# Kernel optimization log

Hardware: AMD Instinct MI355X
Metric: run time of the kernel (lower is better)

Reference implementation:

```python
import jax, jax.numpy as jnp
import numpy as np

B, C, H, W, NH = 16, 384, 28, 28, 6
S = H * W
EPS = 1e-5
SCALE = C ** -0.5  # note: original scales by dim**-0.5, not head_dim**-0.5


def setup_inputs():
    key = jax.random.key(0)
    ks = jax.random.split(key, 5)
    return {
        "x1": jax.random.normal(ks[0], (B, S, C), jnp.float32),
        "h1": H, "w1": W,
        "x2": jax.random.normal(ks[1], (B, S, C), jnp.float32),
        "h2": H, "w2": W,
        # stacked params for the 9 conv branches: q1,k1,v1,q2,k2,v2,q3,k3,v3
        "dw_w": jax.random.normal(ks[2], (9, C, 1, 3, 3), jnp.float32) * 0.1,
        "bn_gamma": jnp.ones((9, C), jnp.float32),
        "bn_beta": jnp.zeros((9, C), jnp.float32),
        "pw_w": jax.random.normal(ks[3], (9, C, C), jnp.float32) * (C ** -0.5),
        "pw_b": jnp.zeros((9, C), jnp.float32),
        "lin_w": jax.random.normal(ks[4], (9, C, C), jnp.float32) * (C ** -0.5),
    }


def _conv_branch(img, dw, g, b, pw, pwb):
    # depthwise 3x3 conv (no bias) -> train-mode BatchNorm2d -> 1x1 conv (bias)
    y = jax.lax.conv_general_dilated(
        img, dw, (1, 1), ((1, 1), (1, 1)),
        feature_group_count=img.shape[1],
        dimension_numbers=('NCHW', 'OIHW', 'NCHW'))
    mu = y.mean(axis=(0, 2, 3), keepdims=True)
    var = ((y - mu) ** 2).mean(axis=(0, 2, 3), keepdims=True)  # biased var, like torch BN
    y = (y - mu) * jax.lax.rsqrt(var + EPS) * g[None, :, None, None] + b[None, :, None, None]
    y = jnp.einsum('bchw,oc->bohw', y, pw) + pwb[None, :, None, None]
    return y.reshape(y.shape[0], y.shape[1], -1).transpose(0, 2, 1)  # b (h w) c


def _heads(x, w):
    # Linear (no bias): y = x @ w.T, then 'b t (h d) -> b h t d'
    y = jnp.einsum('btc,oc->bto', x, w)
    b, t, c = y.shape
    return y.reshape(b, t, NH, c // NH).transpose(0, 2, 1, 3)


def _attn(q, k, v):
    s = jnp.einsum('bhld,bhtd->bhlt', q, k) * SCALE
    a = jax.nn.softmax(s, axis=-1)
    o = jnp.einsum('bhlt,bhtd->bhld', a, v)
    b, h, t, d = o.shape
    # NOTE: original torch does .view(b, t, h*d) on a (b,h,t,d) tensor WITHOUT
    # transposing heads next to depth; replicate that raw reshape exactly.
    return o.reshape(b, t, h * d)


def _forward(x1, h1, w1, x2, h2, w2, dw_w, bn_gamma, bn_beta, pw_w, pw_b, lin_w):
    b, _, c = x1.shape
    i1 = x1.reshape(b, h1, w1, c).transpose(0, 3, 1, 2)  # b c h w
    i2 = x2.reshape(b, h2, w2, c).transpose(0, 3, 1, 2)
    i3 = i1 + i2
    imgs = (i1, i2, i3)
    outs = []
    for br in range(3):
        q = _conv_branch(imgs[br], dw_w[3*br+0], bn_gamma[3*br+0], bn_beta[3*br+0], pw_w[3*br+0], pw_b[3*br+0])
        k = _conv_branch(imgs[br], dw_w[3*br+1], bn_gamma[3*br+1], bn_beta[3*br+1], pw_w[3*br+1], pw_b[3*br+1])
        v = _conv_branch(imgs[br], dw_w[3*br+2], bn_gamma[3*br+2], bn_beta[3*br+2], pw_w[3*br+2], pw_b[3*br+2])
        # branch 3 reuses branch-2 Linear weights (bug in original source, replicated)
        li = 3 if br == 2 else 3 * br
        outs.append(_attn(_heads(q, lin_w[li+0]), _heads(k, lin_w[li+1]), _heads(v, lin_w[li+2])))
    return tuple(outs)


def reference(x1, h1, w1, x2, h2, w2, dw_w, bn_gamma, bn_beta, pw_w, pw_b, lin_w):
    return _forward(x1, h1, w1, x2, h2, w2, dw_w, bn_gamma, bn_beta, pw_w, pw_b, lin_w)
```

## Files before the change

kernel.cpp:

```cpp
#include <hip/hip_runtime.h>

typedef unsigned short u16;
typedef unsigned int u32;
typedef unsigned long long u64;

#define B_   16
#define C_   384
#define H_   28
#define W_   28
#define S_   784
#define NH_  6
#define HD_  64
#define BS_  (B_ * S_)
#define SCALE_ 0.05103103630798288f
#define LSC_   0.07362225484151387f
#define EPS_ 1e-5f

typedef __attribute__((ext_vector_type(8))) short bf16x8;
typedef __attribute__((ext_vector_type(4))) float f32x4;

__device__ __forceinline__ float bf2f(u16 u) {
    return __uint_as_float(((u32)u) << 16);
}
__device__ __forceinline__ u16 f2bf(float f) {
    u32 x = __float_as_uint(f);
    u32 r = (x + 0x7fffu + ((x >> 16) & 1u)) >> 16;
    return (u16)r;
}

__device__ __forceinline__ void gld16(const u16* g, u16* l) {
    __builtin_amdgcn_global_load_lds(
        (__attribute__((address_space(1))) void*)g,
        (__attribute__((address_space(3))) void*)l, 16, 0, 0);
}

__device__ __forceinline__ float exp2_fast(float x) {
    float r;
    asm("v_exp_f32 %0, %1" : "=v"(r) : "v"(x));
    return r;
}

__launch_bounds__(128)
__global__ void k_conv(const float* __restrict__ x1, const float* __restrict__ x2,
                       const float* __restrict__ dw, u16* __restrict__ y,
                       float* __restrict__ part) {
    int id = blockIdx.x;
    int xcd = id & 7;
    int r = id >> 3;
    int cc = r % 3;
    int rr = r / 3;
    int p = xcd + 8 * (rr / 28);
    int h = rr % 28;
    int g = p / 16;
    int b = p % 16;
    int c = cc * 128 + threadIdx.x;

    const float* pa = x1 + (size_t)b * S_ * C_ + c;
    const float* pb = x2 + (size_t)b * S_ * C_ + c;
    float s0 = (g == 1) ? 0.f : 1.f;
    float s1 = (g == 0) ? 0.f : 1.f;

    float wt[3][9];
#pragma unroll
    for (int i = 0; i < 3; ++i)
#pragma unroll
        for (int t = 0; t < 9; ++t)
            wt[i][t] = dw[((3 * g + i) * C_ + c) * 9 + t];

    float rm[3];
    size_t ro[3];
#pragma unroll
    for (int dh = 0; dh < 3; ++dh) {
        int hh = h + dh - 1;
        rm[dh] = (hh >= 0 && hh < H_) ? 1.f : 0.f;
        int hc = hh < 0 ? 0 : (hh > H_ - 1 ? H_ - 1 : hh);
        ro[dh] = (size_t)(hc * W_) * C_;
    }

    float a[3][3];
#pragma unroll
    for (int dh = 0; dh < 3; ++dh) {
        a[dh][0] = 0.f;
        a[dh][1] = (pa[ro[dh]] * s0 + pb[ro[dh]] * s1) * rm[dh];
        a[dh][2] = (pa[ro[dh] + C_] * s0 + pb[ro[dh] + C_] * s1) * rm[dh];
    }

    u16* dst[3];
#pragma unroll
    for (int i = 0; i < 3; ++i)
        dst[i] = y + ((size_t)((3 * g + i) * B_ + b) * S_ + h * W_) * C_ + c;

    float sum[3] = {0.f, 0.f, 0.f}, sq[3] = {0.f, 0.f, 0.f};

#pragma unroll 4
    for (int w = 0; w < W_; ++w) {
        int wn = w + 2;
        float wm = (wn < W_) ? 1.f : 0.f;
        int wc = (wn < W_) ? wn : (W_ - 1);
        size_t o0 = ro[0] + (size_t)wc * C_;
        size_t o1 = ro[1] + (size_t)wc * C_;
        size_t o2 = ro[2] + (size_t)wc * C_;
        float la0 = pa[o0], lb0 = pb[o0];
        float la1 = pa[o1], lb1 = pb[o1];
        float la2 = pa[o2], lb2 = pb[o2];
        float nx0 = (la0 * s0 + lb0 * s1) * (rm[0] * wm);
        float nx1 = (la1 * s0 + lb1 * s1) * (rm[1] * wm);
        float nx2 = (la2 * s0 + lb2 * s1) * (rm[2] * wm);

#pragma unroll
        for (int i = 0; i < 3; ++i) {
            const float* W9 = wt[i];
            float acc = a[0][0]*W9[0] + a[0][1]*W9[1] + a[0][2]*W9[2]
                      + a[1][0]*W9[3] + a[1][1]*W9[4] + a[1][2]*W9[5]
                      + a[2][0]*W9[6] + a[2][1]*W9[7] + a[2][2]*W9[8];
            sum[i] += acc;
            sq[i] = fmaf(acc, acc, sq[i]);
            dst[i][w * C_] = f2bf(acc);
        }
        a[0][0] = a[0][1]; a[0][1] = a[0][2]; a[0][2] = nx0;
        a[1][0] = a[1][1]; a[1][1] = a[1][2]; a[1][2] = nx1;
        a[2][0] = a[2][1]; a[2][1] = a[2][2]; a[2][2] = nx2;
    }
#pragma unroll
    for (int i = 0; i < 3; ++i) {
        atomicAdd(&part[((3 * g + i) * C_ + c) * 2],     sum[i]);
        atomicAdd(&part[((3 * g + i) * C_ + c) * 2 + 1], sq[i]);
    }
}

__global__ void k_wcomb(const float* __restrict__ pw, const float* __restrict__ pwb,
                        const float* __restrict__ lin,
                        const float* __restrict__ part,
                        const float* __restrict__ gamma, const float* __restrict__ beta,
                        u16* __restrict__ Wcb, float* __restrict__ Bc) {
    __shared__ float red[8];
    int id = blockIdx.x;
    int xcd = id & 7;
    int k2 = id >> 3;
    int idx, og;
    if (k2 < 96) { idx = xcd; og = k2; }
    else         { idx = 8;   og = xcd * 12 + (k2 - 96); }
    int c = threadIdx.x;
    int wave = c >> 6, lane = c & 63;
    int li = (idx < 3) ? idx : 3 + (idx % 3);

    float s_ = part[(idx * C_ + c) * 2];
    float q_ = part[(idx * C_ + c) * 2 + 1];
    float mean = s_ / (float)BS_;
    float var  = q_ / (float)BS_ - mean * mean;
    float aS = gamma[idx * C_ + c] * rsqrtf(var + EPS_);
    float bS = beta[idx * C_ + c] - mean * aS;

    float acc[4];
#pragma unroll
    for (int k = 0; k < 4; ++k) acc[k] = 0.f;
    const float* pwm = pw + (idx * C_) * C_ + c;
    const float* lb  = lin + ((li * C_) + og * 4) * C_;

    float pvv[8];
#pragma unroll
    for (int u = 0; u < 8; ++u) pvv[u] = pwm[u * C_];
    for (int m0 = 0; m0 < C_; m0 += 8) {
        float pvn[8];
        if (m0 + 8 < C_) {
#pragma unroll
            for (int u = 0; u < 8; ++u) pvn[u] = pwm[(m0 + 8 + u) * C_];
        } else {
#pragma unroll
            for (int u = 0; u < 8; ++u) pvn[u] = 0.f;
        }
#pragma unroll
        for (int u = 0; u < 8; ++u) {
            float pv = pvv[u];
#pragma unroll
            for (int k = 0; k < 4; ++k)
                acc[k] += lb[k * C_ + (m0 + u)] * pv;
        }
#pragma unroll
        for (int u = 0; u < 8; ++u) pvv[u] = pvn[u];
    }

    float pwbc = pwb[idx * C_ + c];
    for (int k = 0; k < 4; ++k) {
        int o = og * 4 + k;
        Wcb[(idx * C_ + o) * C_ + c] = f2bf(acc[k] * aS);
        float v = acc[k] * bS + lin[(li * C_ + o) * C_ + c] * pwbc;
#pragma unroll
        for (int msk = 1; msk < 64; msk <<= 1) v += __shfl_xor(v, msk);
        if (lane == 0) red[wave] = v;
        __syncthreads();
        if (c == 0)
            Bc[idx * C_ + o] = red[0] + red[1] + red[2] + red[3] + red[4] + red[5];
        __syncthreads();
    }
}

__launch_bounds__(256)
__global__ void k_gemm(const u16* __restrict__ y, const u16* __restrict__ Wcb,
                       const float* __restrict__ Bc, u16* __restrict__ qkv) {
    __shared__ __align__(16) u16 ldsA[2][4096];
    __shared__ __align__(16) u16 ldsB[2][4096];

    int id = blockIdx.x;
    int xcd = id & 7;
    int kb = id >> 3;
    int zz = kb / 21;
    int t  = kb % 21;
    int z  = zz * 8 + xcd;
    int by = t / 7, bx = t % 7;
    int idx = z >> 4, b = z & 15;

    int tid = threadIdx.x;
    int wave = tid >> 6;
    int lane = tid & 63;
    int lq = lane & 15;
    int quad = lane >> 4;
    int o_base = by * 128 + (wave & 1) * 64;
    int s_base_w = bx * 128 + (wave >> 1) * 64;

    const u16* ybase = y + (size_t)(idx * B_ + b) * S_ * C_;
    const u16* wbase = Wcb + (size_t)idx * C_ * C_;

    int r0 = tid >> 2;
    int qs = (tid & 3) ^ ((r0 ^ (r0 >> 2)) & 3);
    int srA0 = bx * 128 + r0;       if (srA0 > S_ - 1) srA0 = S_ - 1;
    int srA1 = bx * 128 + r0 + 64;  if (srA1 > S_ - 1) srA1 = S_ - 1;
    const u16* gA0 = ybase + (size_t)srA0 * C_ + qs * 8;
    const u16* gA1 = ybase + (size_t)srA1 * C_ + qs * 8;
    const u16* gB0 = wbase + (size_t)(by * 128 + r0) * C_ + qs * 8;
    const u16* gB1 = wbase + (size_t)(by * 128 + r0 + 64) * C_ + qs * 8;
    int lo0 = wave * 512;
    int lo1 = 2048 + wave * 512;

#define STAGE(stg, kk) do {                          \
        gld16(gA0 + (kk) * 32, &ldsA[stg][lo0]);     \
        gld16(gA1 + (kk) * 32, &ldsA[stg][lo1]);     \
        gld16(gB0 + (kk) * 32, &ldsB[stg][lo0]);     \
        gld16(gB1 + (kk) * 32, &ldsB[stg][lo1]);     \
    } while (0)

    f32x4 acc[4][4];
#pragma unroll
    for (int i = 0; i < 4; ++i)
#pragma unroll
        for (int j = 0; j < 4; ++j) acc[i][j] = (f32x4){0.f,0.f,0.f,0.f};

    STAGE(0, 0);
    __syncthreads();

    int qoff = (quad ^ ((lq ^ (lq >> 2)) & 3)) * 8;
    bf16x8 af[4], bw[4];
#pragma unroll
    for (int ks = 0; ks < 12; ++ks) {
        int cur = ks & 1;
        if (ks < 11) STAGE(cur ^ 1, ks + 1);
#pragma unroll
        for (int mt = 0; mt < 4; ++mt) {
            int sl = (wave >> 1) * 64 + mt * 16 + lq;
            __builtin_memcpy(&af[mt], &ldsA[cur][sl * 32 + qoff], 16);
        }
#pragma unroll
        for (int nt = 0; nt < 4; ++nt) {
            int ol = (wave & 1) * 64 + nt * 16 + lq;
            __builtin_memcpy(&bw[nt], &ldsB[cur][ol * 32 + qoff], 16);
        }
#pragma unroll
        for (int mt = 0; mt < 4; ++mt)
#pragma unroll
            for (int nt = 0; nt < 4; ++nt)
                acc[mt][nt] = __builtin_amdgcn_mfma_f32_16x16x32_bf16(
                    af[mt], bw[nt], acc[mt][nt], 0, 0, 0);
        __syncthreads();
    }
#undef STAGE

    float bias[4];
#pragma unroll
    for (int nt = 0; nt < 4; ++nt) bias[nt] = Bc[idx * C_ + o_base + nt * 16 + lq];
    u16* obase = qkv + ((size_t)(idx * B_ + b) * S_) * C_;
#pragma unroll
    for (int mt = 0; mt < 4; ++mt) {
#pragma unroll
        for (int r = 0; r < 4; ++r) {
            int s = s_base_w + mt * 16 + quad * 4 + r;
            if (s >= S_) continue;
            u16* row = obase + (size_t)s * C_ + o_base + lq;
#pragma unroll
            for (int nt = 0; nt < 4; ++nt)
                row[nt * 16] = f2bf(acc[mt][nt][r] + bias[nt]);
        }
    }
}

__launch_bounds__(256, 4)
__global__ void k_attn(const u16* __restrict__ qkv, float* __restrict__ out) {
    __shared__ __align__(16) u16 sm[12544];

    int id = blockIdx.x;
    int g8 = id & 7;
    int rest = id >> 3;
    int qtile = rest % 7;
    int zh = (rest / 7) * 8 + g8;
    int z = zh / 6, h = zh % 6;
    int br = z >> 4;
    int tid = threadIdx.x;
    int wave = tid >> 6;
    int lane = tid & 63;
    int lq = lane & 15;
    int quad = lane >> 4;

    int idxq = 3 * br;
    const u16* qp = qkv + (size_t)((idxq * B_ + (z & 15)) * S_) * C_ + h * HD_;
    const u16* kp = qkv + (size_t)(((idxq + 1) * B_ + (z & 15)) * S_) * C_ + h * HD_;
    const u16* vp = qkv + (size_t)(((idxq + 2) * B_ + (z & 15)) * S_) * C_ + h * HD_;

    int qbase = qtile * 128 + wave * 32;
    int qrA = qbase + lq;      if (qrA > S_ - 1) qrA = S_ - 1;
    int qrB = qbase + 16 + lq; if (qrB > S_ - 1) qrB = S_ - 1;
    const u16* qpa = qp + (size_t)qrA * C_ + quad * 8;
    const u16* qpb = qp + (size_t)qrB * C_ + quad * 8;
    bf16x8 aqA0 = *(const bf16x8*)qpa;
    bf16x8 aqA1 = *(const bf16x8*)(qpa + 32);
    bf16x8 aqB0 = *(const bf16x8*)qpb;
    bf16x8 aqB1 = *(const bf16x8*)(qpb + 32);

    f32x4 oA[4], oB[4];
#pragma unroll
    for (int i = 0; i < 4; ++i) { oA[i] = (f32x4){0.f,0.f,0.f,0.f}; oB[i] = oA[i]; }
    float rsA[4] = {0.f,0.f,0.f,0.f}, rsB[4] = {0.f,0.f,0.f,0.f};

    int t2 = (tid & 31) * 2;
    int dg = (tid >> 5) * 8;
    char* smb = (char*)sm;
    u32* pb0 = (u32*)sm + 2048 + wave * 1056;
    u32* pwr = pb0 + (quad * 4) * 66 + lq;
    const u32* prd = pb0 + lq * 66 + quad * 8;
    int sw = lq & 7;
    int vrb0 = lq * 128 + ((quad ^ sw) << 4);
    int vrb1 = lq * 128 + (((4 + quad) ^ sw) << 4);

#define VSTAGE(TG0, TG1) do {                                              \
        bf16x8 v0 = *(const bf16x8*)(vp + (size_t)(TG0) * C_ + dg);        \
        bf16x8 v1 = *(const bf16x8*)(vp + (size_t)(TG1) * C_ + dg);        \
        __syncthreads();                                                   \
        _Pragma("unroll")                                                  \
        for (int e = 0; e < 8; ++e) {                                      \
            u32 pk = (u32)(u16)v0[e] | ((u32)(u16)v1[e] << 16);            \
            *(u32*)(smb + (dg + e) * 128 + ((((t2 >> 3) ^ e)) << 4)        \
                    + ((t2 & 7) << 1)) = pk;                               \
        }                                                                  \
        __syncthreads();                                                   \
    } while (0)

    for (int ch = 0; ch < 12; ++ch) {
        int tc = ch * 64;
        VSTAGE(tc + t2, tc + t2 + 1);

#pragma unroll
        for (int tt = 0; tt < 4; ++tt) {
            const u16* kptr = kp + (size_t)(tc + tt * 16 + lq) * C_ + quad * 8;
            bf16x8 bk0 = *(const bf16x8*)kptr;
            bf16x8 bk1 = *(const bf16x8*)(kptr + 32);
            f32x4 sA = {0.f,0.f,0.f,0.f}, sB = sA;
            sA = __builtin_amdgcn_mfma_f32_16x16x32_bf16(aqA0, bk0, sA, 0, 0, 0);
            sA = __builtin_amdgcn_mfma_f32_16x16x32_bf16(aqA1, bk1, sA, 0, 0, 0);
            sB = __builtin_amdgcn_mfma_f32_16x16x32_bf16(aqB0, bk0, sB, 0, 0, 0);
            sB = __builtin_amdgcn_mfma_f32_16x16x32_bf16(aqB1, bk1, sB, 0, 0, 0);
#pragma unroll
            for (int r = 0; r < 4; ++r) {
                float ea = exp2_fast(sA[r] * LSC_);
                float eb = exp2_fast(sB[r] * LSC_);
                u32 ua = __float_as_uint(ea) & 0xFFFF0000u;
                u32 ub = __float_as_uint(eb) & 0xFFFF0000u;
                rsA[r] += __uint_as_float(ua);
                rsB[r] += __uint_as_float(ub);
                pwr[r * 66 + tt * 16] = __builtin_amdgcn_perm(
                    __float_as_uint(eb), __float_as_uint(ea), 0x07060302u);
            }
        }

        bf16x8 apA[2], apB[2];
#pragma unroll
        for (int n = 0; n < 2; ++n) {
            u32 uu[8];
            __builtin_memcpy(uu, prd + n * 32, 32);
            union { u32 w[4]; bf16x8 v; } ca, cb;
#pragma unroll
            for (int jj = 0; jj < 4; ++jj) {
                ca.w[jj] = __builtin_amdgcn_perm(uu[2*jj+1], uu[2*jj], 0x05040100u);
                cb.w[jj] = __builtin_amdgcn_perm(uu[2*jj+1], uu[2*jj], 0x07060302u);
            }
            apA[n] = ca.v; apB[n] = cb.v;
        }

#pragma unroll
        for (int dt = 0; dt < 4; ++dt) {
            bf16x8 bv0, bv1;
            __builtin_memcpy(&bv0, smb + dt * 2048 + vrb0, 16);
            __builtin_memcpy(&bv1, smb + dt * 2048 + vrb1, 16);
            oA[dt] = __builtin_amdgcn_mfma_f32_16x16x32_bf16(apA[0], bv0, oA[dt], 0, 0, 0);
            oB[dt] = __builtin_amdgcn_mfma_f32_16x16x32_bf16(apB[0], bv0, oB[dt], 0, 0, 0);
            oA[dt] = __builtin_amdgcn_mfma_f32_16x16x32_bf16(apA[1], bv1, oA[dt], 0, 0, 0);
            oB[dt] = __builtin_amdgcn_mfma_f32_16x16x32_bf16(apB[1], bv1, oB[dt], 0, 0, 0);
        }
    }

    {
        int tc = 768;
        int tg0 = tc + t2;     if (tg0 > S_ - 1) tg0 = S_ - 1;
        int tg1 = tc + t2 + 1; if (tg1 > S_ - 1) tg1 = S_ - 1;
        VSTAGE(tg0, tg1);

        const u16* kptr = kp + (size_t)(tc + lq) * C_ + quad * 8;
        bf16x8 bk0 = *(const bf16x8*)kptr;
        bf16x8 bk1 = *(const bf16x8*)(kptr + 32);
        f32x4 sA = {0.f,0.f,0.f,0.f}, sB = sA;
        sA = __builtin_amdgcn_mfma_f32_16x16x32_bf16(aqA0, bk0, sA, 0, 0, 0);
        sA = __builtin_amdgcn_mfma_f32_16x16x32_bf16(aqA1, bk1, sA, 0, 0, 0);
        sB = __builtin_amdgcn_mfma_f32_16x16x32_bf16(aqB0, bk0, sB, 0, 0, 0);
        sB = __builtin_amdgcn_mfma_f32_16x16x32_bf16(aqB1, bk1, sB, 0, 0, 0);
#pragma unroll
        for (int r = 0; r < 4; ++r) {
            float ea = exp2_fast(sA[r] * LSC_);
            float eb = exp2_fast(sB[r] * LSC_);
            u32 ua = __float_as_uint(ea) & 0xFFFF0000u;
            u32 ub = __float_as_uint(eb) & 0xFFFF0000u;
            rsA[r] += __uint_as_float(ua);
            rsB[r] += __uint_as_float(ub);
            pwr[r * 66]      = __builtin_amdgcn_perm(
                __float_as_uint(eb), __float_as_uint(ea), 0x07060302u);
            pwr[r * 66 + 16] = 0;
        }

        bf16x8 apA0, apB0;
        {
            u32 uu[8];
            __builtin_memcpy(uu, prd, 32);
            union { u32 w[4]; bf16x8 v; } ca, cb;
#pragma unroll
            for (int jj = 0; jj < 4; ++jj) {
                ca.w[jj] = __builtin_amdgcn_perm(uu[2*jj+1], uu[2*jj], 0x05040100u);
                cb.w[jj] = __builtin_amdgcn_perm(uu[2*jj+1], uu[2*jj], 0x07060302u);
            }
            apA0 = ca.v; apB0 = cb.v;
        }
#pragma unroll
        for (int dt = 0; dt < 4; ++dt) {
            bf16x8 bv0;
            __builtin_memcpy(&bv0, smb + dt * 2048 + vrb0, 16);
            oA[dt] = __builtin_amdgcn_mfma_f32_16x16x32_bf16(apA0, bv0, oA[dt], 0, 0, 0);
            oB[dt] = __builtin_amdgcn_mfma_f32_16x16x32_bf16(apB0, bv0, oB[dt], 0, 0, 0);
        }
    }
#undef VSTAGE

#pragma unroll
    for (int msk = 1; msk <= 8; msk <<= 1)
#pragma unroll
        for (int r = 0; r < 4; ++r) {
            rsA[r] += __shfl_xor(rsA[r], msk);
            rsB[r] += __shfl_xor(rsB[r], msk);
        }

    size_t obase = ((size_t)z * NH_ + h) * S_ * HD_;
#pragma unroll
    for (int r = 0; r < 4; ++r) {
        int qa = qbase + quad * 4 + r;
        if (qa < S_) {
            float inv = 1.f / rsA[r];
            float* dst = out + obase + (size_t)qa * HD_ + lq;
            dst[0]  = oA[0][r] * inv;
            dst[16] = oA[1][r] * inv;
            dst[32] = oA[2][r] * inv;
            dst[48] = oA[3][r] * inv;
        }
        int qb = qbase + 16 + quad * 4 + r;
        if (qb < S_) {
            float inv = 1.f / rsB[r];
            float* dst = out + obase + (size_t)qb * HD_ + lq;
            dst[0]  = oB[0][r] * inv;
            dst[16] = oB[1][r] * inv;
            dst[32] = oB[2][r] * inv;
            dst[48] = oB[3][r] * inv;
        }
    }
}

extern "C" void kernel_launch(void* const* d_in, const int* in_sizes, int n_in,
                              void* d_out, int out_size, void* d_ws, size_t ws_size,
                              hipStream_t stream) {
    (void)in_sizes; (void)n_in; (void)out_size; (void)ws_size;
    const float* x1    = (const float*)d_in[0];
    const float* x2    = (const float*)d_in[3];
    const float* dw    = (const float*)d_in[6];
    const float* gamma = (const float*)d_in[7];
    const float* beta  = (const float*)d_in[8];
    const float* pw    = (const float*)d_in[9];
    const float* pwb   = (const float*)d_in[10];
    const float* lin   = (const float*)d_in[11];
    float* out = (float*)d_out;

    char* ws = (char*)d_ws;
    u16*  y   = (u16*)(ws + 28901376);
    u16*  qkv = (u16*)(ws + 115605504);
    u16*  Wcb = (u16*)(ws + 202309632);
    float* Bc = (float*)(ws + 204963840);
    float* part = (float*)(ws + 205005312);

    hipMemsetAsync(part, 0, 9 * C_ * 2 * sizeof(float), stream);
    k_conv  <<<dim3(4032), 128, 0, stream>>>(x1, x2, dw, y, part);
    k_wcomb <<<dim3(864), 384, 0, stream>>>(pw, pwb, lin, part, gamma, beta, Wcb, Bc);
    k_gemm  <<<dim3(3024), 256, 0, stream>>>(y, Wcb, Bc, qkv);
    k_attn  <<<dim3(2016), 256, 0, stream>>>(qkv, out);
}
```

Measured before the change: 424.5 us.

## Vectorize depthwise conv to two channels per thread and split BN stats per XCD

The depthwise conv kernel now handles two adjacent channels per thread with float2 loads and packed bf16x2 stores. Blocks grow to 192 threads covering all 384 channels, so the grid shrinks to a third. BN partial sums are accumulated into eight per-XCD copies to cut atomic contention, and k_wcomb sums the eight copies. This trades more registers per thread and fewer blocks for wider memory accesses and fewer contended atomics.

```diff
diff --git a/kernel.cpp b/kernel.cpp
--- a/kernel.cpp
+++ b/kernel.cpp
@@ -18,6 +18,7 @@
 
 typedef __attribute__((ext_vector_type(8))) short bf16x8;
 typedef __attribute__((ext_vector_type(4))) float f32x4;
+typedef __attribute__((ext_vector_type(2))) float f32x2;
 
 __device__ __forceinline__ float bf2f(u16 u) {
     return __uint_as_float(((u32)u) << 16);
@@ -40,91 +41,96 @@
     return r;
 }
 
-__launch_bounds__(128)
+__launch_bounds__(192)
 __global__ void k_conv(const float* __restrict__ x1, const float* __restrict__ x2,
                        const float* __restrict__ dw, u16* __restrict__ y,
                        float* __restrict__ part) {
     int id = blockIdx.x;
     int xcd = id & 7;
-    int r = id >> 3;
-    int cc = r % 3;
-    int rr = r / 3;
-    int p = xcd + 8 * (rr / 28);
-    int h = rr % 28;
+    int j = id >> 3;
+    int p = xcd + 8 * (j / 28);
+    int h = j % 28;
     int g = p / 16;
     int b = p % 16;
-    int c = cc * 128 + threadIdx.x;
-
-    const float* pa = x1 + (size_t)b * S_ * C_ + c;
-    const float* pb = x2 + (size_t)b * S_ * C_ + c;
+    int tid = threadIdx.x;
+    int c0 = tid * 2;
+
+    const f32x2* pa = (const f32x2*)x1 + (size_t)b * S_ * 192 + tid;
+    const f32x2* pb = (const f32x2*)x2 + (size_t)b * S_ * 192 + tid;
     float s0 = (g == 1) ? 0.f : 1.f;
     float s1 = (g == 0) ? 0.f : 1.f;
 
-    float wt[3][9];
+    f32x2 wt[3][9];
 #pragma unroll
     for (int i = 0; i < 3; ++i)
 #pragma unroll
-        for (int t = 0; t < 9; ++t)
-            wt[i][t] = dw[((3 * g + i) * C_ + c) * 9 + t];
+        for (int t = 0; t < 9; ++t) {
+            wt[i][t][0] = dw[((3 * g + i) * C_ + c0) * 9 + t];
+            wt[i][t][1] = dw[((3 * g + i) * C_ + c0 + 1) * 9 + t];
+        }
 
     float rm[3];
-    size_t ro[3];
+    int ro[3];
 #pragma unroll
     for (int dh = 0; dh < 3; ++dh) {
         int hh = h + dh - 1;
         rm[dh] = (hh >= 0 && hh < H_) ? 1.f : 0.f;
         int hc = hh < 0 ? 0 : (hh > H_ - 1 ? H_ - 1 : hh);
-        ro[dh] = (size_t)(hc * W_) * C_;
-    }
-
-    float a[3][3];
+        ro[dh] = hc * W_ * 192;
+    }
+
+    f32x2 a[3][3];
 #pragma unroll
     for (int dh = 0; dh < 3; ++dh) {
-        a[dh][0] = 0.f;
-        a[dh][1] = (pa[ro[dh]] * s0 + pb[ro[dh]] * s1) * rm[dh];
-        a[dh][2] = (pa[ro[dh] + C_] * s0 + pb[ro[dh] + C_] * s1) * rm[dh];
-    }
-
-    u16* dst[3];
+        f32x2 v1 = pa[ro[dh]],       w1 = pb[ro[dh]];
+        f32x2 v2 = pa[ro[dh] + 192], w2 = pb[ro[dh] + 192];
+        a[dh][0] = (f32x2){0.f, 0.f};
+        a[dh][1] = (v1 * s0 + w1 * s1) * rm[dh];
+        a[dh][2] = (v2 * s0 + w2 * s1) * rm[dh];
+    }
+
+    u32* du[3];
 #pragma unroll
     for (int i = 0; i < 3; ++i)
-        dst[i] = y + ((size_t)((3 * g + i) * B_ + b) * S_ + h * W_) * C_ + c;
-
-    float sum[3] = {0.f, 0.f, 0.f}, sq[3] = {0.f, 0.f, 0.f};
+        du[i] = (u32*)(y + ((size_t)((3 * g + i) * B_ + b) * S_ + h * W_) * C_ + c0);
+
+    f32x2 sum[3], sq[3];
+#pragma unroll
+    for (int i = 0; i < 3; ++i) { sum[i] = (f32x2){0.f, 0.f}; sq[i] = sum[i]; }
 
 #pragma unroll 4
     for (int w = 0; w < W_; ++w) {
         int wn = w + 2;
         float wm = (wn < W_) ? 1.f : 0.f;
         int wc = (wn < W_) ? wn : (W_ - 1);
-        size_t o0 = ro[0] + (size_t)wc * C_;
-        size_t o1 = ro[1] + (size_t)wc * C_;
-        size_t o2 = ro[2] + (size_t)wc * C_;
-        float la0 = pa[o0], lb0 = pb[o0];
-        float la1 = pa[o1], lb1 = pb[o1];
-        float la2 = pa[o2], lb2 = pb[o2];
-        float nx0 = (la0 * s0 + lb0 * s1) * (rm[0] * wm);
-        float nx1 = (la1 * s0 + lb1 * s1) * (rm[1] * wm);
-        float nx2 = (la2 * s0 + lb2 * s1) * (rm[2] * wm);
+        f32x2 la0 = pa[ro[0] + wc * 192], lb0 = pb[ro[0] + wc * 192];
+        f32x2 la1 = pa[ro[1] + wc * 192], lb1 = pb[ro[1] + wc * 192];
+        f32x2 la2 = pa[ro[2] + wc * 192], lb2 = pb[ro[2] + wc * 192];
+        f32x2 nx0 = (la0 * s0 + lb0 * s1) * (rm[0] * wm);
+        f32x2 nx1 = (la1 * s0 + lb1 * s1) * (rm[1] * wm);
+        f32x2 nx2 = (la2 * s0 + lb2 * s1) * (rm[2] * wm);
 
 #pragma unroll
         for (int i = 0; i < 3; ++i) {
-            const float* W9 = wt[i];
-            float acc = a[0][0]*W9[0] + a[0][1]*W9[1] + a[0][2]*W9[2]
-                      + a[1][0]*W9[3] + a[1][1]*W9[4] + a[1][2]*W9[5]
-                      + a[2][0]*W9[6] + a[2][1]*W9[7] + a[2][2]*W9[8];
+            f32x2 acc = a[0][0]*wt[i][0] + a[0][1]*wt[i][1] + a[0][2]*wt[i][2]
+                      + a[1][0]*wt[i][3] + a[1][1]*wt[i][4] + a[1][2]*wt[i][5]
+                      + a[2][0]*wt[i][6] + a[2][1]*wt[i][7] + a[2][2]*wt[i][8];
             sum[i] += acc;
-            sq[i] = fmaf(acc, acc, sq[i]);
-            dst[i][w * C_] = f2bf(acc);
+            sq[i] += acc * acc;
+            u32 pk = (u32)f2bf(acc[0]) | ((u32)f2bf(acc[1]) << 16);
+            du[i][w * 192] = pk;
         }
         a[0][0] = a[0][1]; a[0][1] = a[0][2]; a[0][2] = nx0;
         a[1][0] = a[1][1]; a[1][1] = a[1][2]; a[1][2] = nx1;
         a[2][0] = a[2][1]; a[2][1] = a[2][2]; a[2][2] = nx2;
     }
+    float* ps = part + xcd * (9 * C_ * 2);
 #pragma unroll
     for (int i = 0; i < 3; ++i) {
-        atomicAdd(&part[((3 * g + i) * C_ + c) * 2],     sum[i]);
-        atomicAdd(&part[((3 * g + i) * C_ + c) * 2 + 1], sq[i]);
+        atomicAdd(&ps[((3 * g + i) * C_ + c0) * 2],         sum[i][0]);
+        atomicAdd(&ps[((3 * g + i) * C_ + c0) * 2 + 1],     sq[i][0]);
+        atomicAdd(&ps[((3 * g + i) * C_ + c0 + 1) * 2],     sum[i][1]);
+        atomicAdd(&ps[((3 * g + i) * C_ + c0 + 1) * 2 + 1], sq[i][1]);
     }
 }
 
@@ -144,8 +150,12 @@
     int wave = c >> 6, lane = c & 63;
     int li = (idx < 3) ? idx : 3 + (idx % 3);
 
-    float s_ = part[(idx * C_ + c) * 2];
-    float q_ = part[(idx * C_ + c) * 2 + 1];
+    float s_ = 0.f, q_ = 0.f;
+#pragma unroll
+    for (int x = 0; x < 8; ++x) {
+        s_ += part[x * (9 * C_ * 2) + (idx * C_ + c) * 2];
+        q_ += part[x * (9 * C_ * 2) + (idx * C_ + c) * 2 + 1];
+    }
     float mean = s_ / (float)BS_;
     float var  = q_ / (float)BS_ - mean * mean;
     float aS = gamma[idx * C_ + c] * rsqrtf(var + EPS_);
@@ -243,7 +253,7 @@
 #pragma unroll
     for (int i = 0; i < 4; ++i)
 #pragma unroll
-        for (int j = 0; j < 4; ++j) acc[i][j] = (f32x4){0.f,0.f,0.f,0.f};
+        for (int j2 = 0; j2 < 4; ++j2) acc[i][j2] = (f32x4){0.f,0.f,0.f,0.f};
 
     STAGE(0, 0);
     __syncthreads();
@@ -501,14 +511,14 @@
     float* out = (float*)d_out;
 
     char* ws = (char*)d_ws;
+    float* part = (float*)(ws + 0);
     u16*  y   = (u16*)(ws + 28901376);
     u16*  qkv = (u16*)(ws + 115605504);
     u16*  Wcb = (u16*)(ws + 202309632);
     float* Bc = (float*)(ws + 204963840);
-    float* part = (float*)(ws + 205005312);
-
-    hipMemsetAsync(part, 0, 9 * C_ * 2 * sizeof(float), stream);
-    k_conv  <<<dim3(4032), 128, 0, stream>>>(x1, x2, dw, y, part);
+
+    hipMemsetAsync(part, 0, 8 * 9 * C_ * 2 * sizeof(float), stream);
+    k_conv  <<<dim3(1344), 192, 0, stream>>>(x1, x2, dw, y, part);
     k_wcomb <<<dim3(864), 384, 0, stream>>>(pw, pwb, lin, part, gamma, beta, Wcb, Bc);
     k_gemm  <<<dim3(3024), 256, 0, stream>>>(y, Wcb, Bc, qkv);
     k_attn  <<<dim3(2016), 256, 0, stream>>>(qkv, out);
```

Result: faster. 412.0 us (-2.9%).
